# Optimization experiments

Hardware: AMD Instinct MI355X
Metric: run time of the kernel (lower is better)

## Reference

```python
import jax, jax.numpy as jnp
import numpy as np

L, B, H, NI, V = 256, 32, 1024, 1024, 10000


def setup_inputs() -> dict:
    key = jax.random.key(0)
    ks = jax.random.split(key, 8)
    return {
        "input_ids": jax.random.randint(ks[0], (L, B), 0, V),
        "h0": jnp.zeros((B, H), jnp.float32),
        "c0": jnp.zeros((B, H), jnp.float32),
        "emb_w": jax.random.uniform(ks[1], (V, NI), jnp.float32, -0.1, 0.1),
        "w_ih": jax.random.normal(ks[2], (4 * H, NI), jnp.float32) * 0.02,
        "w_hh": jax.random.normal(ks[3], (4 * H, H), jnp.float32) * 0.02,
        "dec_w": jax.random.uniform(ks[4], (V, H), jnp.float32, -0.1, 0.1),
        "dec_b": jnp.zeros((V,), jnp.float32),
        "W": jax.random.normal(ks[5], (H, 1), jnp.float32) * 0.1,
        "U": jax.random.normal(ks[6], (H, 1), jnp.float32) * 0.1,
    }


def reference(input_ids, h0, c0, emb_w, w_ih, w_hh, dec_w, dec_b, W, U):
    seq_len, bsz = input_ids.shape
    nhid = h0.shape[1]
    emb = emb_w[input_ids]  # [L, B, NI]

    def lstm_cell(x, h, c):
        # torch LSTMCell (bias=False), gate order i, f, g, o
        gates = x @ w_ih.T + h @ w_hh.T  # [B, 4H]
        i, f, g, o = jnp.split(gates, 4, axis=-1)
        c_new = jax.nn.sigmoid(f) * c + jax.nn.sigmoid(i) * jnp.tanh(g)
        h_new = jax.nn.sigmoid(o) * jnp.tanh(c_new)
        return h_new, c_new

    time_idx = jnp.arange(seq_len)

    def step(carry, xs):
        h, c, hist = carry  # hist: [L, B, H] padded history of hiddens
        x, i = xs
        h, c = lstm_cell(x, h, c)
        hist = hist.at[i].set(h)
        # additive attention over all hiddens so far
        b = (hist.reshape(-1, nhid) @ U).reshape(seq_len, bsz)  # [L, B]
        a = (h @ W).reshape(1, bsz)  # [1, B]
        scores = jnp.tanh(a + b)
        scores = jnp.where((time_idx <= i)[:, None], scores, -jnp.inf)
        att = jax.nn.softmax(scores, axis=0)  # softmax over time
        ctx = jnp.sum(att[:, :, None] * hist, axis=0)  # [B, H]
        return (h, c, hist), ctx

    hist0 = jnp.zeros((seq_len, bsz, nhid), dtype=h0.dtype)
    (h, c, _), ctx = jax.lax.scan(step, (h0, c0, hist0), (emb, time_idx))
    # ctx: [L, B, H]
    logits = ctx @ dec_w.T + dec_b  # [L, B, V]
    out = jax.nn.log_softmax(logits, axis=-1)
    return out, (h, c)
```

## Files before the change

### kernel.cpp

```cpp
#include <hip/hip_runtime.h>
#include <math.h>

typedef unsigned short u16;
typedef unsigned u32;
typedef float f32x4 __attribute__((ext_vector_type(4)));
typedef float f32x2 __attribute__((ext_vector_type(2)));
typedef __bf16 bf16x8 __attribute__((ext_vector_type(8)));
typedef u16 u16x8 __attribute__((ext_vector_type(8)));
typedef u16 u16x4 __attribute__((ext_vector_type(4)));
typedef u32 u32x4 __attribute__((ext_vector_type(4)));

#define L_SEQ 256
#define BSZ 32
#define HID 1024
#define NIN 1024
#define VOC 10000
#define G4 4096
#define MROWS 8192
#define NB 64
#define DPB 16
#define SENT 0xFFFFFFFFu

__device__ __forceinline__ u16 f2bf(float f) {
    unsigned u = __float_as_uint(f);
    unsigned r = u + 0x7FFFu + ((u >> 16) & 1u);
    return (u16)(r >> 16);
}
#define BF2F(x) __builtin_bit_cast(float, (u32)((u16)(x)) << 16)

__device__ __forceinline__ float fast_sigm(float x) {
    x = fminf(fmaxf(x, -15.f), 15.f);
    return __builtin_amdgcn_rcpf(1.f + __expf(-x));
}
__device__ __forceinline__ float fast_tanh(float x) {
    x = fminf(fmaxf(x, -15.f), 15.f);
    float t = __expf(2.f * x);
    return (t - 1.f) * __builtin_amdgcn_rcpf(t + 1.f);
}
__device__ __forceinline__ unsigned umax4(u16x8 v) {
    u32x4 c = __builtin_bit_cast(u32x4, v);
    unsigned a = c.x > c.y ? c.x : c.y;
    unsigned b = c.z > c.w ? c.z : c.w;
    return a > b ? a : b;
}

__global__ __launch_bounds__(256) void cvt_bf16_kernel(const float* __restrict__ in,
                                                       u16* __restrict__ out, int n4) {
    int idx = blockIdx.x * 256 + threadIdx.x;
    if (idx < n4) {
        f32x4 v = *(const f32x4*)(in + (size_t)idx * 4);
        u16x4 o = {f2bf(v.x), f2bf(v.y), f2bf(v.z), f2bf(v.w)};
        *(u16x4*)(out + (size_t)idx * 4) = o;
    }
}

__global__ __launch_bounds__(256) void gather_emb_kernel(const int* __restrict__ ids,
                                                         const float* __restrict__ emb_w,
                                                         u16* __restrict__ out) {
    int m = blockIdx.x;
    int id = ids[m];
    const float* src = emb_w + (size_t)id * NIN;
    u16* dst = out + (size_t)m * NIN;
    int t = threadIdx.x;
    f32x4 v = *(const f32x4*)(src + t * 4);
    u16x4 o = {f2bf(v.x), f2bf(v.y), f2bf(v.z), f2bf(v.w)};
    *(u16x4*)(dst + t * 4) = o;
}

__global__ __launch_bounds__(256) void gemm_gxT_kernel(const u16* __restrict__ A,
                                                       const u16* __restrict__ B,
                                                       float* __restrict__ gxT) {
    int m0 = blockIdx.x * 128;
    int n0 = blockIdx.y * 128;
    __shared__ alignas(16) u16 As[128][40];
    __shared__ alignas(16) u16 Bs[128][40];
    int t = threadIdx.x;
    int lane = t & 63, wave = t >> 6;
    int wr = wave >> 1, wc = wave & 1;
    int l15 = lane & 15, l4 = lane >> 4;

    f32x4 acc[4][4];
    f32x4 zv = {0.f, 0.f, 0.f, 0.f};
    for (int mi = 0; mi < 4; ++mi)
        for (int ni = 0; ni < 4; ++ni) acc[mi][ni] = zv;

    for (int k0 = 0; k0 < NIN; k0 += 32) {
        for (int s = 0; s < 2; ++s) {
            int task = t + s * 256;
            int row = task >> 2, kof = (task & 3) * 8;
            *(u16x8*)(&As[row][kof]) = *(const u16x8*)(A + (size_t)(m0 + row) * NIN + k0 + kof);
            *(u16x8*)(&Bs[row][kof]) = *(const u16x8*)(B + (size_t)(n0 + row) * NIN + k0 + kof);
        }
        __syncthreads();
        bf16x8 af[4], bfr[4];
        for (int mi = 0; mi < 4; ++mi)
            af[mi] = __builtin_bit_cast(bf16x8, *(const u16x8*)(&As[wr * 64 + mi * 16 + l15][l4 * 8]));
        for (int ni = 0; ni < 4; ++ni)
            bfr[ni] = __builtin_bit_cast(bf16x8, *(const u16x8*)(&Bs[wc * 64 + ni * 16 + l15][l4 * 8]));
        for (int mi = 0; mi < 4; ++mi)
            for (int ni = 0; ni < 4; ++ni)
                acc[mi][ni] = __builtin_amdgcn_mfma_f32_16x16x32_bf16(af[mi], bfr[ni], acc[mi][ni], 0, 0, 0);
        __syncthreads();
    }
    for (int mi = 0; mi < 4; ++mi)
        for (int ni = 0; ni < 4; ++ni) {
            int n = n0 + wc * 64 + ni * 16 + l15;
            int g = n >> 10, dd = n & 1023;
            int dblk = dd >> 4, dl = dd & 15;
            int mbase = m0 + wr * 64 + mi * 16 + l4 * 4;
            int i = mbase >> 5, bb = mbase & 31;
            size_t idx = ((((size_t)dblk * L_SEQ + i) * 4 + g) * 16 + dl) * 32 + bb;
            *(f32x4*)(&gxT[idx]) = acc[mi][ni];
        }
}

__global__ __launch_bounds__(256) void gemm_bt_kernel(const u16* __restrict__ A,
                                                      const u16* __restrict__ B,
                                                      float* __restrict__ C,
                                                      const float* __restrict__ bias,
                                                      int M, int N, int K) {
    int m0 = blockIdx.x * 128;
    int n0 = blockIdx.y * 128;
    __shared__ alignas(16) u16 As[128][40];
    __shared__ alignas(16) u16 Bs[128][40];
    int t = threadIdx.x;
    int lane = t & 63, wave = t >> 6;
    int wr = wave >> 1, wc = wave & 1;
    int l15 = lane & 15, l4 = lane >> 4;

    f32x4 acc[4][4];
    f32x4 zv = {0.f, 0.f, 0.f, 0.f};
    for (int mi = 0; mi < 4; ++mi)
        for (int ni = 0; ni < 4; ++ni) acc[mi][ni] = zv;

    for (int k0 = 0; k0 < K; k0 += 32) {
        for (int s = 0; s < 2; ++s) {
            int task = t + s * 256;
            int row = task >> 2, kof = (task & 3) * 8;
            u16x8 av = *(const u16x8*)(A + (size_t)(m0 + row) * K + k0 + kof);
            *(u16x8*)(&As[row][kof]) = av;
            int brow = n0 + row;
            u16x8 bv = {0, 0, 0, 0, 0, 0, 0, 0};
            if (brow < N) bv = *(const u16x8*)(B + (size_t)brow * K + k0 + kof);
            *(u16x8*)(&Bs[row][kof]) = bv;
        }
        __syncthreads();
        bf16x8 af[4], bfr[4];
        for (int mi = 0; mi < 4; ++mi)
            af[mi] = __builtin_bit_cast(bf16x8, *(const u16x8*)(&As[wr * 64 + mi * 16 + l15][l4 * 8]));
        for (int ni = 0; ni < 4; ++ni)
            bfr[ni] = __builtin_bit_cast(bf16x8, *(const u16x8*)(&Bs[wc * 64 + ni * 16 + l15][l4 * 8]));
        for (int mi = 0; mi < 4; ++mi)
            for (int ni = 0; ni < 4; ++ni)
                acc[mi][ni] = __builtin_amdgcn_mfma_f32_16x16x32_bf16(af[mi], bfr[ni], acc[mi][ni], 0, 0, 0);
        __syncthreads();
    }

    for (int mi = 0; mi < 4; ++mi)
        for (int ni = 0; ni < 4; ++ni) {
            int col = n0 + wc * 64 + ni * 16 + l15;
            if (col < N) {
                float bb = bias ? bias[col] : 0.f;
                int rbase = m0 + wr * 64 + mi * 16 + l4 * 4;
                for (int r = 0; r < 4; ++r)
                    C[(size_t)(rbase + r) * N + col] = acc[mi][ni][r] + bb;
            }
        }
}

__global__ __launch_bounds__(256, 1) void lstm_seq_kernel(
    const float* __restrict__ c0, const u16* __restrict__ w_hh_bf,
    const float* __restrict__ gxT, const float* __restrict__ Wv, const float* __restrict__ Uv,
    u16* __restrict__ hb_hist, float* __restrict__ out_tail, float* __restrict__ part_ab) {
    __shared__ alignas(16) u16 Bs[64][1024];
    __shared__ float gsm[4][32][16];
    __shared__ float c_sl[32][16];

    int blk = blockIdx.x;
    int d0 = blk * DPB;
    int t = threadIdx.x;
    int lane = t & 63, wave = t >> 6;
    int wm = wave & 1, wn = wave >> 1;
    int l15 = lane & 15, l4 = lane >> 4;

    for (int s = 0; s < 32; ++s) {
        int cid = t + s * 256;
        int c = cid >> 7;
        int ch = cid & 127;
        int g = c >> 4, dl = c & 15;
        u16x8 v = *(const u16x8*)(w_hh_bf + (size_t)(g * HID + d0 + dl) * HID + ch * 8);
        int chs = ch ^ (c & 7);
        *(u16x8*)(&Bs[c][chs * 8]) = v;
    }
    for (int s = t; s < 512; s += 256) {
        int b = s >> 4, dl = s & 15;
        c_sl[b][dl] = c0[b * HID + d0 + dl];
    }
    __syncthreads();

    int cA = wn * 32 + l15;
    int cB = cA + 16;
    int sw = cA & 7;
    int gA = cA >> 4, dA = cA & 15;
    int gB = cB >> 4, dB = cB & 15;

    int bb = t >> 3;
    int pr = t & 7;
    int dl0 = pr * 2;

    const float* gxTb = gxT + (size_t)blk * ((size_t)L_SEQ * 2048) + wm * 16 + l4 * 4;

    for (int i = 0; i < L_SEQ; ++i) {
        const u16* hb = hb_hist + (size_t)i * (BSZ * HID);
        const u16* aptr = hb + (size_t)(wm * 16 + l15) * HID + l4 * 8;

        f32x4 gxa0 = *(const f32x4*)(gxTb + (size_t)i * 2048 + gA * 512 + dA * 32);
        f32x4 gxa1 = *(const f32x4*)(gxTb + (size_t)i * 2048 + gB * 512 + dB * 32);

        u16x8 afr[32];
        unsigned needmask = 0xFFFFFFFFu;
        do {
#pragma unroll
            for (int kk = 0; kk < 32; ++kk)
                if (needmask & (1u << kk))
                    asm volatile("global_load_dwordx4 %0, %1, off offset:%c2 sc0 sc1"
                                 : "=v"(afr[kk])
                                 : "v"(aptr), "n"(kk * 64));
            asm volatile("s_waitcnt vmcnt(0)" ::: "memory");
            __builtin_amdgcn_sched_barrier(0);
            unsigned nm = 0;
#pragma unroll
            for (int kk = 0; kk < 32; ++kk)
                if (needmask & (1u << kk)) {
                    if (__ballot(umax4(afr[kk]) == SENT)) nm |= (1u << kk);
                }
            needmask = nm;
            if (needmask) __builtin_amdgcn_s_sleep(1);
        } while (needmask);
        __builtin_amdgcn_sched_barrier(0);

        f32x4 acc0 = {0.f, 0.f, 0.f, 0.f}, acc1 = {0.f, 0.f, 0.f, 0.f};
#pragma unroll
        for (int kk = 0; kk < 32; ++kk) {
            bf16x8 af = __builtin_bit_cast(bf16x8, afr[kk]);
            int ch = kk * 4 + l4;
            bf16x8 b0 = __builtin_bit_cast(bf16x8, *(const u16x8*)(&Bs[cA][(ch ^ sw) * 8]));
            bf16x8 b1 = __builtin_bit_cast(bf16x8, *(const u16x8*)(&Bs[cB][(ch ^ sw) * 8]));
            acc0 = __builtin_amdgcn_mfma_f32_16x16x32_bf16(af, b0, acc0, 0, 0, 0);
            acc1 = __builtin_amdgcn_mfma_f32_16x16x32_bf16(af, b1, acc1, 0, 0, 0);
        }

#pragma unroll
        for (int r = 0; r < 4; ++r) {
            int m = wm * 16 + l4 * 4 + r;
            gsm[gA][m][dA] = acc0[r] + gxa0[r];
            gsm[gB][m][dB] = acc1[r] + gxa1[r];
        }
        __syncthreads();

        u16* hb_next = hb_hist + (size_t)(i + 1) * (BSZ * HID);
        float hn01[2];
#pragma unroll
        for (int q = 0; q < 2; ++q) {
            int dl = dl0 + q;
            float ig = gsm[0][bb][dl], fg = gsm[1][bb][dl];
            float gg = gsm[2][bb][dl], og = gsm[3][bb][dl];
            float cn = fast_sigm(fg) * c_sl[bb][dl] + fast_sigm(ig) * fast_tanh(gg);
            float hn = fast_sigm(og) * fast_tanh(cn);
            c_sl[bb][dl] = cn;
            hn01[q] = hn;
        }
        unsigned pk = (unsigned)f2bf(hn01[0]) | ((unsigned)f2bf(hn01[1]) << 16);
        __hip_atomic_store((unsigned*)(hb_next + bb * HID + d0 + dl0), pk,
                           __ATOMIC_RELAXED, __HIP_MEMORY_SCOPE_AGENT);
        if (i == L_SEQ - 1) {
            f32x2 hv = {hn01[0], hn01[1]};
            *(f32x2*)(out_tail + (size_t)bb * HID + d0 + dl0) = hv;
        }
        float pa = hn01[0] * Wv[d0 + dl0] + hn01[1] * Wv[d0 + dl0 + 1];
        float pb = hn01[0] * Uv[d0 + dl0] + hn01[1] * Uv[d0 + dl0 + 1];
        pa += __shfl_xor(pa, 1); pb += __shfl_xor(pb, 1);
        pa += __shfl_xor(pa, 2); pb += __shfl_xor(pb, 2);
        pa += __shfl_xor(pa, 4); pb += __shfl_xor(pb, 4);
        if (pr == 0) {
            f32x2 pv = {pa, pb};
            *(f32x2*)(part_ab + (((size_t)i * NB + blk) * BSZ + bb) * 2) = pv;
        }
    }

    for (int s = t; s < 512; s += 256) {
        int b2 = s >> 4, dl = s & 15;
        out_tail[(size_t)BSZ * HID + b2 * HID + d0 + dl] = c_sl[b2][dl];
    }
}

__global__ __launch_bounds__(256) void reduce_ab_kernel(const float* __restrict__ part_ab,
                                                        float* __restrict__ a_arr,
                                                        float* __restrict__ b_arr) {
    int i = blockIdx.x;
    int t = threadIdx.x;
    int b = t & 31, q = t >> 5;
    float sa = 0.f, sb = 0.f;
    for (int j = 0; j < 8; ++j) {
        int blk = q * 8 + j;
        f32x2 v = *(const f32x2*)(part_ab + (((size_t)i * NB + blk) * BSZ + b) * 2);
        sa += v.x;
        sb += v.y;
    }
    __shared__ float ra[8][32], rb[8][32];
    ra[q][b] = sa;
    rb[q][b] = sb;
    __syncthreads();
    if (q == 0) {
        for (int j = 1; j < 8; ++j) { sa += ra[j][b]; sb += rb[j][b]; }
        a_arr[i * BSZ + b] = sa;
        b_arr[i * BSZ + b] = sb;
    }
}

__global__ __launch_bounds__(256) void attn_kernel(const float* __restrict__ a_arr,
                                                   const float* __restrict__ b_arr,
                                                   const u16* __restrict__ hb_hist,
                                                   u16* __restrict__ ctx_bf) {
    int b = blockIdx.y;
    int i0 = blockIdx.x * 8;
    int t = threadIdx.x;
    __shared__ float att[8][256];
    __shared__ float red[256];

    float bt = b_arr[t * BSZ + b];
    for (int q = 0; q < 8; ++q) {
        int iq = i0 + q;
        att[q][t] = (t <= iq) ? tanhf(a_arr[iq * BSZ + b] + bt) : -INFINITY;
    }
    __syncthreads();
    for (int q = 0; q < 8; ++q) {
        int iq = i0 + q;
        red[t] = att[q][t];
        __syncthreads();
        for (int s = 128; s > 0; s >>= 1) {
            if (t < s) red[t] = fmaxf(red[t], red[t + s]);
            __syncthreads();
        }
        float m = red[0];
        __syncthreads();
        float e = (t <= iq) ? expf(att[q][t] - m) : 0.f;
        red[t] = e;
        __syncthreads();
        for (int s = 128; s > 0; s >>= 1) {
            if (t < s) red[t] += red[t + s];
            __syncthreads();
        }
        float sum = red[0];
        __syncthreads();
        att[q][t] = e / sum;
        __syncthreads();
    }

    int hc = t * 4;
    f32x4 accq[8];
    f32x4 zv = {0.f, 0.f, 0.f, 0.f};
    for (int q = 0; q < 8; ++q) accq[q] = zv;
    int imax = i0 + 7;
    for (int t2 = 0; t2 <= imax; ++t2) {
        u16x4 hq = *(const u16x4*)(hb_hist + (size_t)(t2 + 1) * (BSZ * HID) + (size_t)b * HID + hc);
        f32x4 hv = {BF2F(hq.x), BF2F(hq.y), BF2F(hq.z), BF2F(hq.w)};
        for (int q = 0; q < 8; ++q) accq[q] += hv * att[q][t2];
    }
    for (int q = 0; q < 8; ++q) {
        size_t row = (size_t)(i0 + q) * BSZ + b;
        u16x4 o = {f2bf(accq[q].x), f2bf(accq[q].y), f2bf(accq[q].z), f2bf(accq[q].w)};
        *(u16x4*)(ctx_bf + row * HID + hc) = o;
    }
}

__global__ __launch_bounds__(256) void logsoftmax_kernel(float* __restrict__ x, int V) {
    int row = blockIdx.x;
    float* p = x + (size_t)row * V;
    __shared__ float red[256];
    int t = threadIdx.x;
    float frag[40];
    float m = -INFINITY;
#pragma unroll
    for (int k = 0; k < 40; ++k) {
        int j = t + k * 256;
        if (j < VOC) {
            frag[k] = p[j];
            m = fmaxf(m, frag[k]);
        }
    }
    red[t] = m;
    __syncthreads();
    for (int s = 128; s > 0; s >>= 1) {
        if (t < s) red[t] = fmaxf(red[t], red[t + s]);
        __syncthreads();
    }
    m = red[0];
    __syncthreads();
    float sum = 0.f;
#pragma unroll
    for (int k = 0; k < 40; ++k) {
        int j = t + k * 256;
        if (j < VOC) sum += __expf(frag[k] - m);
    }
    red[t] = sum;
    __syncthreads();
    for (int s = 128; s > 0; s >>= 1) {
        if (t < s) red[t] += red[t + s];
        __syncthreads();
    }
    float lse = m + logf(red[0]);
#pragma unroll
    for (int k = 0; k < 40; ++k) {
        int j = t + k * 256;
        if (j < VOC) p[j] = frag[k] - lse;
    }
}

extern "C" void kernel_launch(void* const* d_in, const int* in_sizes, int n_in,
                              void* d_out, int out_size, void* d_ws, size_t ws_size,
                              hipStream_t stream) {
    const int* ids = (const int*)d_in[0];
    const float* h0 = (const float*)d_in[1];
    const float* c0 = (const float*)d_in[2];
    const float* emb_w = (const float*)d_in[3];
    const float* w_ih = (const float*)d_in[4];
    const float* w_hh = (const float*)d_in[5];
    const float* dec_w = (const float*)d_in[6];
    const float* dec_b = (const float*)d_in[7];
    const float* Wv = (const float*)d_in[8];
    const float* Uv = (const float*)d_in[9];

    char* p = (char*)d_ws;
    auto alloc = [&](size_t bytes) {
        void* r = (void*)p;
        p += (bytes + 255) & ~(size_t)255;
        return r;
    };
    u16* w_ih_bf = (u16*)alloc((size_t)G4 * NIN * 2);
    u16* w_hh_bf = (u16*)alloc((size_t)G4 * HID * 2);
    u16* dec_w_bf = (u16*)alloc((size_t)VOC * HID * 2);
    char* hbreg = (char*)alloc((size_t)(L_SEQ + 1) * BSZ * HID * 2);
    u16* ctx_bf = (u16*)alloc((size_t)MROWS * HID * 2);
    float* part_ab = (float*)alloc((size_t)L_SEQ * NB * BSZ * 2 * 4);
    float* a_arr = (float*)alloc((size_t)L_SEQ * BSZ * 4);
    float* b_arr = (float*)alloc((size_t)L_SEQ * BSZ * 4);

    u16* A_emb = (u16*)hbreg;
    u16* hb_hist = (u16*)hbreg;
    float* out = (float*)d_out;
    float* gxT = out;
    float* out_tail = out + (size_t)MROWS * VOC;

    cvt_bf16_kernel<<<G4 * NIN / 1024, 256, 0, stream>>>(w_ih, w_ih_bf, G4 * NIN / 4);
    cvt_bf16_kernel<<<G4 * HID / 1024, 256, 0, stream>>>(w_hh, w_hh_bf, G4 * HID / 4);
    cvt_bf16_kernel<<<(VOC * HID / 4 + 255) / 256, 256, 0, stream>>>(dec_w, dec_w_bf, VOC * HID / 4);
    gather_emb_kernel<<<MROWS, 256, 0, stream>>>(ids, emb_w, A_emb);
    gemm_gxT_kernel<<<dim3(MROWS / 128, G4 / 128), 256, 0, stream>>>(A_emb, w_ih_bf, gxT);

    hipMemsetAsync(hb_hist + (size_t)BSZ * HID, 0xFF, (size_t)L_SEQ * BSZ * HID * 2, stream);
    cvt_bf16_kernel<<<BSZ * HID / 1024, 256, 0, stream>>>(h0, hb_hist, BSZ * HID / 4);

    {
        const float* c0a = c0;
        const u16* whha = w_hh_bf;
        const float* gxa = gxT;
        const float* Wa = Wv;
        const float* Ua = Uv;
        u16* hba = hb_hist;
        float* tail = out_tail;
        float* pab = part_ab;
        void* args[] = {&c0a, &whha, &gxa, &Wa, &Ua, &hba, &tail, &pab};
        hipLaunchCooperativeKernel((const void*)lstm_seq_kernel, dim3(NB), dim3(256), args, 0,
                                   stream);
    }
    reduce_ab_kernel<<<L_SEQ, 256, 0, stream>>>(part_ab, a_arr, b_arr);
    attn_kernel<<<dim3(L_SEQ / 8, BSZ), 256, 0, stream>>>(a_arr, b_arr, hb_hist, ctx_bf);
    gemm_bt_kernel<<<dim3(MROWS / 128, (VOC + 127) / 128), 256, 0, stream>>>(ctx_bf, dec_w_bf, out,
                                                                             dec_b, MROWS, VOC, HID);
    logsoftmax_kernel<<<MROWS, 256, 0, stream>>>(out, VOC);
}
```

Baseline: 2.587 ms.

## Consume ready h chunks with MFMA during spin-wait and prefetch next gate inputs

The recurrent LSTM loop now issues all 32 h-fragment loads up front and runs the MFMA on each chunk as soon as its sentinel clears, re-polling only the pending chunks instead of waiting for the whole row before computing. The per-step gx input loads are prefetched at the end of the previous iteration so their latency overlaps the step tail. Shared gate and cell buffers are padded to 17 columns to avoid LDS bank conflicts. The cost is more complex control flow inside the unrolled loop and possible register pressure from the predicated MFMAs.

```diff
diff --git a/kernel.cpp b/kernel.cpp
--- a/kernel.cpp
+++ b/kernel.cpp
@@ -173,8 +173,8 @@
     const float* __restrict__ gxT, const float* __restrict__ Wv, const float* __restrict__ Uv,
     u16* __restrict__ hb_hist, float* __restrict__ out_tail, float* __restrict__ part_ab) {
     __shared__ alignas(16) u16 Bs[64][1024];
-    __shared__ float gsm[4][32][16];
-    __shared__ float c_sl[32][16];
+    __shared__ float gsm[4][32][17];
+    __shared__ float c_sl[32][17];
 
     int blk = blockIdx.x;
     int d0 = blk * DPB;
@@ -210,45 +210,51 @@
 
     const float* gxTb = gxT + (size_t)blk * ((size_t)L_SEQ * 2048) + wm * 16 + l4 * 4;
 
+    f32x4 gxa0 = *(const f32x4*)(gxTb + (size_t)0 * 2048 + gA * 512 + dA * 32);
+    f32x4 gxa1 = *(const f32x4*)(gxTb + (size_t)0 * 2048 + gB * 512 + dB * 32);
+
     for (int i = 0; i < L_SEQ; ++i) {
         const u16* hb = hb_hist + (size_t)i * (BSZ * HID);
         const u16* aptr = hb + (size_t)(wm * 16 + l15) * HID + l4 * 8;
 
-        f32x4 gxa0 = *(const f32x4*)(gxTb + (size_t)i * 2048 + gA * 512 + dA * 32);
-        f32x4 gxa1 = *(const f32x4*)(gxTb + (size_t)i * 2048 + gB * 512 + dB * 32);
-
         u16x8 afr[32];
-        unsigned needmask = 0xFFFFFFFFu;
-        do {
+#pragma unroll
+        for (int kk = 0; kk < 32; ++kk)
+            asm volatile("global_load_dwordx4 %0, %1, off offset:%c2 sc0 sc1"
+                         : "=v"(afr[kk])
+                         : "v"(aptr), "n"(kk * 64));
+
+        f32x4 acc0 = {0.f, 0.f, 0.f, 0.f}, acc1 = {0.f, 0.f, 0.f, 0.f};
+        unsigned pend = 0xFFFFFFFFu;
+        for (;;) {
+            asm volatile("s_waitcnt vmcnt(0)" ::: "memory");
+            __builtin_amdgcn_sched_barrier(0);
+            unsigned done = 0;
+#pragma unroll
+            for (int kk = 0; kk < 32; ++kk) {
+                if (pend & (1u << kk)) {
+                    if (__ballot(umax4(afr[kk]) == SENT) == 0) {
+                        bf16x8 af = __builtin_bit_cast(bf16x8, afr[kk]);
+                        int ch = kk * 4 + l4;
+                        bf16x8 b0 = __builtin_bit_cast(bf16x8, *(const u16x8*)(&Bs[cA][(ch ^ sw) * 8]));
+                        bf16x8 b1 = __builtin_bit_cast(bf16x8, *(const u16x8*)(&Bs[cB][(ch ^ sw) * 8]));
+                        acc0 = __builtin_amdgcn_mfma_f32_16x16x32_bf16(af, b0, acc0, 0, 0, 0);
+                        acc1 = __builtin_amdgcn_mfma_f32_16x16x32_bf16(af, b1, acc1, 0, 0, 0);
+                        done |= 1u << kk;
+                    }
+                }
+            }
+            pend &= ~done;
+            if (!pend) break;
 #pragma unroll
             for (int kk = 0; kk < 32; ++kk)
-                if (needmask & (1u << kk))
+                if (pend & (1u << kk))
                     asm volatile("global_load_dwordx4 %0, %1, off offset:%c2 sc0 sc1"
                                  : "=v"(afr[kk])
                                  : "v"(aptr), "n"(kk * 64));
-            asm volatile("s_waitcnt vmcnt(0)" ::: "memory");
-            __builtin_amdgcn_sched_barrier(0);
-            unsigned nm = 0;
-#pragma unroll
-            for (int kk = 0; kk < 32; ++kk)
-                if (needmask & (1u << kk)) {
-                    if (__ballot(umax4(afr[kk]) == SENT)) nm |= (1u << kk);
-                }
-            needmask = nm;
-            if (needmask) __builtin_amdgcn_s_sleep(1);
-        } while (needmask);
+            __builtin_amdgcn_s_sleep(1);
+        }
         __builtin_amdgcn_sched_barrier(0);
-
-        f32x4 acc0 = {0.f, 0.f, 0.f, 0.f}, acc1 = {0.f, 0.f, 0.f, 0.f};
-#pragma unroll
-        for (int kk = 0; kk < 32; ++kk) {
-            bf16x8 af = __builtin_bit_cast(bf16x8, afr[kk]);
-            int ch = kk * 4 + l4;
-            bf16x8 b0 = __builtin_bit_cast(bf16x8, *(const u16x8*)(&Bs[cA][(ch ^ sw) * 8]));
-            bf16x8 b1 = __builtin_bit_cast(bf16x8, *(const u16x8*)(&Bs[cB][(ch ^ sw) * 8]));
-            acc0 = __builtin_amdgcn_mfma_f32_16x16x32_bf16(af, b0, acc0, 0, 0, 0);
-            acc1 = __builtin_amdgcn_mfma_f32_16x16x32_bf16(af, b1, acc1, 0, 0, 0);
-        }
 
 #pragma unroll
         for (int r = 0; r < 4; ++r) {
@@ -286,6 +292,10 @@
             f32x2 pv = {pa, pb};
             *(f32x2*)(part_ab + (((size_t)i * NB + blk) * BSZ + bb) * 2) = pv;
         }
+
+        int inx = (i + 1 < L_SEQ) ? i + 1 : i;
+        gxa0 = *(const f32x4*)(gxTb + (size_t)inx * 2048 + gA * 512 + dA * 32);
+        gxa1 = *(const f32x4*)(gxTb + (size_t)inx * 2048 + gB * 512 + dB * 32);
     }
 
     for (int s = t; s < 512; s += 256) {
```

Measured after the change: 2.605 ms. Within noise of the previous version (+0.7%).
